# Kernel optimization log

Measured on AMD Instinct MI355X. Metric: run time of the kernel, lower is better.

## Reference

```python
import jax, jax.numpy as jnp
import numpy as np

B, S, D_IN, D_OUT, H = 2, 2048, 1024, 1024, 16
HD = D_OUT // H  # head dim = 64


def setup_inputs() -> dict:
    key = jax.random.key(0)
    ks = jax.random.split(key, 9)
    s_in = 1.0 / np.sqrt(D_IN)
    s_out = 1.0 / np.sqrt(D_OUT)
    return {
        "X": jax.random.normal(ks[0], (B, S, D_IN), dtype=jnp.float32),
        "Wq": jax.random.uniform(ks[1], (D_OUT, D_IN), jnp.float32, -s_in, s_in),
        "bq": jax.random.uniform(ks[2], (D_OUT,), jnp.float32, -s_in, s_in),
        "Wk": jax.random.uniform(ks[3], (D_OUT, D_IN), jnp.float32, -s_in, s_in),
        "bk": jax.random.uniform(ks[4], (D_OUT,), jnp.float32, -s_in, s_in),
        "Wv": jax.random.uniform(ks[5], (D_OUT, D_IN), jnp.float32, -s_in, s_in),
        "bv": jax.random.uniform(ks[6], (D_OUT,), jnp.float32, -s_in, s_in),
        "Wo": jax.random.uniform(ks[7], (D_OUT, D_OUT), jnp.float32, -s_out, s_out),
        "bo": jax.random.uniform(ks[8], (D_OUT,), jnp.float32, -s_out, s_out),
    }


def reference(X, Wq, bq, Wk, bk, Wv, bv, Wo, bo):
    scale = jnp.asarray(HD ** 0.5, X.dtype)  # self.dim = sqrt(head_dim)
    q = X @ Wq.T + bq  # [B,S,D_OUT]
    k = X @ Wk.T + bk
    v = X @ Wv.T + bv
    # split heads: b s (h d) -> b h s d
    q = q.reshape(B, S, H, HD).transpose(0, 2, 1, 3)
    k = k.reshape(B, S, H, HD).transpose(0, 2, 1, 3)
    v = v.reshape(B, S, H, HD).transpose(0, 2, 1, 3)
    scores = jnp.einsum('bhsd,bhtd->bhst', q, k) / scale  # [B,H,S,S]
    causal = jnp.triu(jnp.ones((S, S), dtype=bool), k=1)
    scores = jnp.where(causal, -jnp.inf, scores)
    weights = jax.nn.softmax(scores, axis=-1)
    out = jnp.einsum('bhst,bhtd->bhsd', weights, v)  # [B,H,S,HD]
    out = out.transpose(0, 2, 1, 3).reshape(B, S, D_OUT)  # b h s d -> b s (h d)
    return out @ Wo.T + bo
```

## Files before the change

kernel.cpp:

```cpp
#include <hip/hip_runtime.h>
#include <hip/hip_bf16.h>

typedef __bf16 bf16_t;
typedef __bf16 bf16x8 __attribute__((ext_vector_type(8)));
typedef float  f32x4  __attribute__((ext_vector_type(4)));
typedef unsigned short ushort_t;

#define MFMA16(a, b, c) __builtin_amdgcn_mfma_f32_16x16x32_bf16((a), (b), (c), 0, 0, 0)
#define GLDS16(g, l) __builtin_amdgcn_global_load_lds( \
    (const __attribute__((address_space(1))) unsigned int*)(g), \
    (__attribute__((address_space(3))) unsigned int*)(l), 16, 0, 0)

#define WAITCNT_VM(n)  (0x0F70 | (n))
#define WAITCNT_LGKM0  0xC07F

#define MEMFENCE asm volatile("" ::: "memory")

#define SWZ(r) ((((r) >> 1) ^ ((r) >> 3)) & 3)

#define QSCALE 0.18033688f

__global__ __launch_bounds__(256) void cvt_all(
    const void* __restrict__ X,  const void* __restrict__ W0, const void* __restrict__ W1,
    const void* __restrict__ W2, const void* __restrict__ W3,
    const void* __restrict__ c0, const void* __restrict__ c1,
    const void* __restrict__ c2, const void* __restrict__ c3,
    bf16_t* __restrict__ Xb, bf16_t* __restrict__ Wb, float* __restrict__ biasF,
    int* __restrict__ flag)
{
    const int tid  = threadIdx.x;
    const int lane = tid & 63;
    const ushort_t u = ((const ushort_t*)X)[2 * lane];
    const int e = (u >> 7) & 0xFF;
    const int f = (__ballot(e >= 0xA0) != 0ull) ? 1 : 0;

    const int bid = blockIdx.x;
    if (bid >= 4096) {
        if (bid == 4096 && tid == 0) *flag = f;
        const int idx = ((bid - 4096) * 256 + tid) * 8;
        const int w = idx >> 10, off = idx & 1023;
        const void* src = (w == 0) ? c0 : (w == 1) ? c1 : (w == 2) ? c2 : c3;
        #pragma unroll
        for (int r = 0; r < 8; ++r)
            biasF[idx + r] = f ? ((const float*)src)[off + r]
                               : (float)((const bf16_t*)src)[off + r];
        return;
    }

    const long long i = (long long)bid * 2048 + tid * 8;
    const void* src;
    bf16_t* dst;
    long long off;
    if (i < 4194304) { src = X; dst = Xb; off = i; }
    else {
        const int w = (int)((i - 4194304) >> 20);
        off = (i - 4194304) & 1048575;
        src = (w == 0) ? W0 : (w == 1) ? W1 : (w == 2) ? W2 : W3;
        dst = Wb + (size_t)w * 1048576;
    }
    if (f) {
        const float* s = (const float*)src + off;
        const float4 a = *(const float4*)(s);
        const float4 b = *(const float4*)(s + 4);
        bf16x8 o;
        o[0] = (bf16_t)a.x; o[1] = (bf16_t)a.y; o[2] = (bf16_t)a.z; o[3] = (bf16_t)a.w;
        o[4] = (bf16_t)b.x; o[5] = (bf16_t)b.y; o[6] = (bf16_t)b.z; o[7] = (bf16_t)b.w;
        *(bf16x8*)(dst + off) = o;
    } else {
        *(bf16x8*)(dst + off) = *(const bf16x8*)((const bf16_t*)src + off);
    }
}

__global__ __launch_bounds__(512, 2) void gemm_qkv(
    const bf16_t* __restrict__ A,
    const bf16_t* __restrict__ Wst,
    const float* __restrict__ biasAll,
    bf16_t* __restrict__ C, bf16_t* __restrict__ Vt)
{
    __shared__ bf16_t Ash[4][256 * 32];
    __shared__ bf16_t Bsh[4][192 * 32];

    const int tid  = threadIdx.x;
    const int wid  = tid >> 6;
    const int lane = tid & 63;
    const int g    = lane >> 4;
    const int c    = lane & 15;

    const int m0 = blockIdx.x * 256;
    const int n0 = blockIdx.y * 192;

    const int srow = lane >> 2;
    const int sblk = (lane & 3) ^ ((lane >> 3) & 3);
    const bf16_t* Ag  = A   + (size_t)(m0 + wid * 32 + srow) * 1024 + sblk * 8;
    const bf16_t* Wg0 = Wst + (size_t)(n0 + wid * 16 + srow) * 1024 + sblk * 8;
    const bf16_t* Wg1 = Wst + (size_t)(n0 + 128 + wid * 16 + srow) * 1024 + sblk * 8;

    const int waveM = (wid >> 2) * 128;
    const int waveN = (wid & 3) * 48;
    const int fblk  = (g ^ ((c >> 1) & 3)) * 8;

    f32x4 acc[8][3] = {};

    auto stage = [&](int H) {
        const int buf = H & 3;
        GLDS16(Ag + H * 32,                      &Ash[buf][(wid * 32) * 32]);
        GLDS16(Ag + (size_t)16 * 1024 + H * 32,  &Ash[buf][(wid * 32 + 16) * 32]);
        GLDS16(Wg0 + H * 32,                     &Bsh[buf][(wid * 16) * 32]);
        if (wid < 4)
            GLDS16(Wg1 + H * 32,                 &Bsh[buf][(128 + wid * 16) * 32]);
    };

    stage(0); stage(1); stage(2);
    if (wid < 4) __builtin_amdgcn_s_waitcnt(WAITCNT_VM(8));
    else         __builtin_amdgcn_s_waitcnt(WAITCNT_VM(6));
    __builtin_amdgcn_s_barrier();
    MEMFENCE;

    #pragma unroll 4
    for (int H = 0; H < 32; ++H) {
        const int buf = H & 3;
        const bf16_t* As = Ash[buf];
        const bf16_t* Bs = Bsh[buf];

        bf16x8 bfr[3], af[8];
        #pragma unroll
        for (int j = 0; j < 3; ++j)
            bfr[j] = *(const bf16x8*)(&Bs[(waveN + j * 16 + c) * 32 + fblk]);
        #pragma unroll
        for (int i = 0; i < 8; ++i)
            af[i] = *(const bf16x8*)(&As[(waveM + i * 16 + c) * 32 + fblk]);

        if (H < 29) stage(H + 3);

        __builtin_amdgcn_s_setprio(1);
        #pragma unroll
        for (int i = 0; i < 8; ++i)
            #pragma unroll
            for (int j = 0; j < 3; ++j)
                acc[i][j] = MFMA16(af[i], bfr[j], acc[i][j]);
        __builtin_amdgcn_s_setprio(0);

        MEMFENCE;
        __builtin_amdgcn_s_waitcnt(WAITCNT_LGKM0);
        if (H < 29) {
            if (wid < 4) __builtin_amdgcn_s_waitcnt(WAITCNT_VM(8));
            else         __builtin_amdgcn_s_waitcnt(WAITCNT_VM(6));
        } else if (H == 29) {
            if (wid < 4) __builtin_amdgcn_s_waitcnt(WAITCNT_VM(4));
            else         __builtin_amdgcn_s_waitcnt(WAITCNT_VM(3));
        } else if (H == 30) {
            __builtin_amdgcn_s_waitcnt(WAITCNT_VM(0));
        }
        __builtin_amdgcn_s_barrier();
        MEMFENCE;
    }

    #pragma unroll
    for (int j = 0; j < 3; ++j) {
        const int cg0 = n0 + waveN + j * 16;
        const int col = cg0 + c;
        const float bv = biasAll[col];
        if (cg0 >= 2048) {
            const int hcol = col - 2048;
            const int h = hcol >> 6, d = hcol & 63;
            #pragma unroll
            for (int i = 0; i < 8; ++i) {
                const int row = m0 + waveM + i * 16 + g * 4;
                const int bb = row >> 11, s = row & 2047;
                bf16_t pk[4];
                #pragma unroll
                for (int r = 0; r < 4; ++r) pk[r] = (bf16_t)(acc[i][j][r] + bv);
                *(uint2*)(&Vt[(((size_t)bb * 16 + h) * 64 + d) * 2048 + s]) = *(uint2*)pk;
            }
        } else {
            const float os = (cg0 < 1024) ? QSCALE : 1.0f;
            #pragma unroll
            for (int i = 0; i < 8; ++i) {
                const int row = m0 + waveM + i * 16 + g * 4;
                #pragma unroll
                for (int r = 0; r < 4; ++r)
                    C[(size_t)(row + r) * 3072 + col] = (bf16_t)((acc[i][j][r] + bv) * os);
            }
        }
    }
}

template<int TM>
__global__ __launch_bounds__(256, 3) void gemm_nt(
    const bf16_t* __restrict__ A,
    const bf16_t* __restrict__ W0,
    const float* __restrict__ b0,
    void* __restrict__ C, int ldc,
    const int* __restrict__ flag, int is_out)
{
    constexpr int MI = TM / 32;
    __shared__ bf16_t Ash[2][TM * 32];
    __shared__ bf16_t Bsh[2][128 * 32];

    const int f32out = is_out ? *flag : 0;

    const int tid  = threadIdx.x;
    const int wid  = tid >> 6;
    const int lane = tid & 63;
    const int g    = lane >> 4;
    const int c    = lane & 15;

    const int m0  = blockIdx.x * TM;
    const int n0  = blockIdx.y * 128;
    const bf16_t* W  = W0;
    const float*  bs = b0;
    const int nw = n0 & 1023;

    const int srow = lane >> 2;
    const int sblk = (lane & 3) ^ ((lane >> 3) & 3);
    const bf16_t* Ag = A + (size_t)(m0 + wid * (TM / 4) + srow) * 1024 + sblk * 8;
    const bf16_t* Wg = W + (size_t)(nw + wid * 32 + srow) * 1024 + sblk * 8;

    const int waveM = (wid >> 1) * (TM / 2);
    const int waveN = (wid & 1) * 64;

    f32x4 acc[MI][4] = {};
    const int fblk = (g ^ ((c >> 1) & 3)) * 8;

    auto stage = [&](int t) {
        const int k0 = t * 32;
        const int buf = t & 1;
        bf16_t* As = &Ash[buf][(wid * (TM / 4)) * 32];
        bf16_t* Bs = &Bsh[buf][(wid * 32) * 32];
        GLDS16(Ag + k0, As);
        if (TM == 128) GLDS16(Ag + (size_t)16 * 1024 + k0, As + 16 * 32);
        GLDS16(Wg + k0, Bs);
        GLDS16(Wg + (size_t)16 * 1024 + k0, Bs + 16 * 32);
    };

    stage(0);
    __builtin_amdgcn_s_waitcnt(WAITCNT_VM(0));
    __builtin_amdgcn_s_barrier();
    MEMFENCE;

    #pragma unroll 2
    for (int k = 0; k < 32; ++k) {
        const int cur = k & 1;
        bf16x8 af[MI], bfr[4];
        #pragma unroll
        for (int i = 0; i < MI; ++i)
            af[i] = *(const bf16x8*)(&Ash[cur][(waveM + i * 16 + c) * 32 + fblk]);
        #pragma unroll
        for (int j = 0; j < 4; ++j)
            bfr[j] = *(const bf16x8*)(&Bsh[cur][(waveN + j * 16 + c) * 32 + fblk]);

        if (k < 31) stage(k + 1);

        __builtin_amdgcn_s_setprio(1);
        #pragma unroll
        for (int i = 0; i < MI; ++i)
            #pragma unroll
            for (int j = 0; j < 4; ++j)
                acc[i][j] = MFMA16(af[i], bfr[j], acc[i][j]);
        __builtin_amdgcn_s_setprio(0);

        MEMFENCE;
        __builtin_amdgcn_s_waitcnt(WAITCNT_LGKM0);
        if (k < 31) __builtin_amdgcn_s_waitcnt(WAITCNT_VM(0));
        __builtin_amdgcn_s_barrier();
        MEMFENCE;
    }

    #pragma unroll
    for (int j = 0; j < 4; ++j) {
        const int col = n0 + waveN + j * 16 + c;
        const float bv = bs[col & 1023];
        #pragma unroll
        for (int i = 0; i < MI; ++i) {
            const int row = m0 + waveM + i * 16 + g * 4;
            #pragma unroll
            for (int r = 0; r < 4; ++r) {
                const float val = acc[i][j][r] + bv;
                const size_t idx = (size_t)(row + r) * ldc + col;
                if (f32out) ((float*)C)[idx] = val;
                else        ((bf16_t*)C)[idx] = (bf16_t)val;
            }
        }
    }
}

__global__ __launch_bounds__(256, 4) void attn_kernel(
    const bf16_t* __restrict__ QKV, const bf16_t* __restrict__ Vt,
    bf16_t* __restrict__ O)
{
    __shared__ bf16_t Ksh[2][64][32];
    __shared__ bf16_t Vsh[2][64][32];
    __shared__ bf16_t Psh[4][16][72];

    const int tid  = threadIdx.x;
    const int wid  = tid >> 6;
    const int lane = tid & 63;
    const int g    = lane >> 4;
    const int c    = lane & 15;

    const int bh = blockIdx.y;
    const int b  = bh >> 4, h = bh & 15;
    const int qt = (bh < 16) ? blockIdx.x : (31 - blockIdx.x);
    const int q0 = qt * 64;
    const int nt = qt + 1;

    bf16x8 aq[2];
    {
        const bf16_t* qp = QKV + (size_t)(b * 2048 + q0 + wid * 16 + c) * 3072 + h * 64;
        aq[0] = *(const bf16x8*)(qp + g * 8);
        aq[1] = *(const bf16x8*)(qp + 32 + g * 8);
    }

    float li = 0.0f;
    f32x4 o2[4] = {};

    const int sr = tid >> 2;
    const int j4 = tid & 3;
    const bf16_t* Kg = QKV + (size_t)(b * 2048 + sr) * 3072 + 1024 + h * 64 + j4 * 8;
    const bf16_t* Vg = Vt + ((size_t)bh * 64 + sr) * 2048 + j4 * 8;

    const int sp = (j4 ^ SWZ(sr)) * 8;
    bf16_t* kd0 = &Ksh[0][sr][sp];
    bf16_t* kd1 = &Ksh[1][sr][sp];
    bf16_t* vd0 = &Vsh[0][sr][sp];
    bf16_t* vd1 = &Vsh[1][sr][sp];

    uint4 kr0 = *(const uint4*)(Kg);
    uint4 kr1 = *(const uint4*)(Kg + 32);
    uint4 vr0 = *(const uint4*)(Vg);
    uint4 vr1 = *(const uint4*)(Vg + 32);

    const int qg = q0 + wid * 16 + c;

    for (int jt = 0; jt < nt; ++jt) {
        *(uint4*)kd0 = kr0;
        *(uint4*)kd1 = kr1;
        *(uint4*)vd0 = vr0;
        *(uint4*)vd1 = vr1;
        __syncthreads();

        if (jt + 1 < nt) {
            const size_t ko = (size_t)(jt + 1) * 64 * 3072;
            kr0 = *(const uint4*)(Kg + ko);
            kr1 = *(const uint4*)(Kg + ko + 32);
            vr0 = *(const uint4*)(Vg + (jt + 1) * 64);
            vr1 = *(const uint4*)(Vg + (jt + 1) * 64 + 32);
        }

        f32x4 s[4] = {};
        __builtin_amdgcn_s_setprio(1);
        #pragma unroll
        for (int n = 0; n < 4; ++n)
            #pragma unroll
            for (int kb = 0; kb < 2; ++kb) {
                const int row = n * 16 + c;
                const bf16x8 kf = *(const bf16x8*)(&Ksh[kb][row][(g ^ SWZ(row)) * 8]);
                s[n] = MFMA16(kf, aq[kb], s[n]);
            }
        __builtin_amdgcn_s_setprio(0);

        if (jt == nt - 1) {
            const int j0 = jt * 64;
            #pragma unroll
            for (int n = 0; n < 4; ++n)
                #pragma unroll
                for (int r = 0; r < 4; ++r)
                    if (j0 + n * 16 + g * 4 + r > qg) s[n][r] = -1e30f;
        }

        #pragma unroll
        for (int n = 0; n < 4; ++n) {
            const float p0 = __builtin_amdgcn_exp2f(s[n][0]);
            const float p1 = __builtin_amdgcn_exp2f(s[n][1]);
            const float p2 = __builtin_amdgcn_exp2f(s[n][2]);
            const float p3 = __builtin_amdgcn_exp2f(s[n][3]);
            li += (p0 + p1) + (p2 + p3);
            union { bf16_t h[4]; uint2 u; } pk;
            pk.h[0] = (bf16_t)p0; pk.h[1] = (bf16_t)p1;
            pk.h[2] = (bf16_t)p2; pk.h[3] = (bf16_t)p3;
            const int pw = ((n ^ (c >> 2)) << 2) + (g ^ (c & 3));
            *(uint2*)(&Psh[wid][c][pw * 4]) = pk.u;
        }
        __builtin_amdgcn_wave_barrier();

        bf16x8 pb[2];
        #pragma unroll
        for (int kb = 0; kb < 2; ++kb) {
            const int n0  = 2 * kb + (g >> 1);
            const int gs  = (g & 1) * 2;
            const int base = ((n0 ^ (c >> 2)) << 2);
            const uint2 w0 = *(const uint2*)(&Psh[wid][c][(base + (gs ^ (c & 3))) * 4]);
            const uint2 w1 = *(const uint2*)(&Psh[wid][c][(base + ((gs + 1) ^ (c & 3))) * 4]);
            union { uint4 u; bf16x8 v; } cvt;
            cvt.u.x = w0.x; cvt.u.y = w0.y; cvt.u.z = w1.x; cvt.u.w = w1.y;
            pb[kb] = cvt.v;
        }

        __builtin_amdgcn_s_setprio(1);
        #pragma unroll
        for (int kb = 0; kb < 2; ++kb)
            #pragma unroll
            for (int dt = 0; dt < 4; ++dt) {
                const int row = dt * 16 + c;
                const bf16x8 vf = *(const bf16x8*)(&Vsh[kb][row][(g ^ SWZ(row)) * 8]);
                o2[dt] = MFMA16(vf, pb[kb], o2[dt]);
            }
        __builtin_amdgcn_s_setprio(0);
        __syncthreads();
    }

    li += __shfl_xor(li, 16, 64);
    li += __shfl_xor(li, 32, 64);
    const float inv = 1.0f / li;

    const size_t orow = (size_t)(b * 2048 + q0 + wid * 16 + c);
    #pragma unroll
    for (int dt = 0; dt < 4; ++dt) {
        union { bf16_t h[4]; uint2 u; } pk;
        #pragma unroll
        for (int r = 0; r < 4; ++r) pk.h[r] = (bf16_t)(o2[dt][r] * inv);
        *(uint2*)(&O[orow * 1024 + h * 64 + dt * 16 + g * 4]) = pk.u;
    }
}

extern "C" void kernel_launch(void* const* d_in, const int* in_sizes, int n_in,
                              void* d_out, int out_size, void* d_ws, size_t ws_size,
                              hipStream_t stream)
{
    const void* X  = d_in[0];
    const void* Wq = d_in[1];  const void* bq = d_in[2];
    const void* Wk = d_in[3];  const void* bk = d_in[4];
    const void* Wv = d_in[5];  const void* bv = d_in[6];
    const void* Wo = d_in[7];  const void* bo = d_in[8];

    int*    flag  = (int*)d_ws;
    float*  biasF = (float*)((char*)d_ws + 16);
    bf16_t* Xb    = (bf16_t*)((char*)d_ws + 16 + 16384);
    bf16_t* Wb    = Xb  + (size_t)4096 * 1024;
    bf16_t* QKV   = Wb  + (size_t)4 * 1024 * 1024;
    bf16_t* Vt    = QKV + (size_t)4096 * 3072;
    bf16_t* Ao    = Vt  + (size_t)4096 * 1024;

    const size_t MW = (size_t)1024 * 1024;

    cvt_all<<<4098, 256, 0, stream>>>(X, Wq, Wk, Wv, Wo, bq, bk, bv, bo,
                                      Xb, Wb, biasF, flag);

    gemm_qkv<<<dim3(16, 16), 512, 0, stream>>>(Xb, Wb, biasF, QKV, Vt);
    attn_kernel<<<dim3(32, 32), 256, 0, stream>>>(QKV, Vt, Ao);
    gemm_nt<64><<<dim3(64, 8), 256, 0, stream>>>(
        Ao, Wb + 3 * MW, biasF + 3072, d_out, 1024, flag, 1);
}
```

Measured before the change: 194.8 us.

## Rewrite output projection GEMM with 128x128 tiles, 512 threads, triple-buffered K=64 stages

Replaces the templated 64x128-tile output GEMM with a dedicated kernel using 128x128 tiles and 8 waves. It loads K in 64-wide stages into a three-deep LDS ring, keeping two stages in flight. The goal is to raise data reuse per tile and hide global-load latency with fewer barriers. The cost is a grid of only 256 blocks, which may underfill the device's CUs, plus much larger LDS use per block.

```diff
diff --git a/kernel.cpp b/kernel.cpp
--- a/kernel.cpp
+++ b/kernel.cpp
@@ -185,19 +185,17 @@
     }
 }
 
-template<int TM>
-__global__ __launch_bounds__(256, 3) void gemm_nt(
+__global__ __launch_bounds__(512, 1) void gemm_op(
     const bf16_t* __restrict__ A,
-    const bf16_t* __restrict__ W0,
-    const float* __restrict__ b0,
-    void* __restrict__ C, int ldc,
-    const int* __restrict__ flag, int is_out)
+    const bf16_t* __restrict__ W,
+    const float* __restrict__ bs,
+    void* __restrict__ C,
+    const int* __restrict__ flag)
 {
-    constexpr int MI = TM / 32;
-    __shared__ bf16_t Ash[2][TM * 32];
-    __shared__ bf16_t Bsh[2][128 * 32];
-
-    const int f32out = is_out ? *flag : 0;
+    __shared__ bf16_t As[3][2][128 * 32];
+    __shared__ bf16_t Bs[3][2][128 * 32];
+
+    const int f32out = *flag;
 
     const int tid  = threadIdx.x;
     const int wid  = tid >> 6;
@@ -205,78 +203,77 @@
     const int g    = lane >> 4;
     const int c    = lane & 15;
 
-    const int m0  = blockIdx.x * TM;
-    const int n0  = blockIdx.y * 128;
-    const bf16_t* W  = W0;
-    const float*  bs = b0;
-    const int nw = n0 & 1023;
+    const int m0 = blockIdx.x * 128;
+    const int n0 = blockIdx.y * 128;
 
     const int srow = lane >> 2;
     const int sblk = (lane & 3) ^ ((lane >> 3) & 3);
-    const bf16_t* Ag = A + (size_t)(m0 + wid * (TM / 4) + srow) * 1024 + sblk * 8;
-    const bf16_t* Wg = W + (size_t)(nw + wid * 32 + srow) * 1024 + sblk * 8;
-
-    const int waveM = (wid >> 1) * (TM / 2);
-    const int waveN = (wid & 1) * 64;
-
-    f32x4 acc[MI][4] = {};
-    const int fblk = (g ^ ((c >> 1) & 3)) * 8;
+    const bf16_t* Ag = A + (size_t)(m0 + wid * 16 + srow) * 1024 + sblk * 8;
+    const bf16_t* Wg = W + (size_t)(n0 + wid * 16 + srow) * 1024 + sblk * 8;
+
+    const int waveM = (wid >> 2) * 64;
+    const int waveN = (wid & 3) * 32;
+    const int fblk  = (g ^ ((c >> 1) & 3)) * 8;
+
+    f32x4 acc[4][2] = {};
 
     auto stage = [&](int t) {
-        const int k0 = t * 32;
-        const int buf = t & 1;
-        bf16_t* As = &Ash[buf][(wid * (TM / 4)) * 32];
-        bf16_t* Bs = &Bsh[buf][(wid * 32) * 32];
-        GLDS16(Ag + k0, As);
-        if (TM == 128) GLDS16(Ag + (size_t)16 * 1024 + k0, As + 16 * 32);
-        GLDS16(Wg + k0, Bs);
-        GLDS16(Wg + (size_t)16 * 1024 + k0, Bs + 16 * 32);
+        const int buf = t % 3;
+        const size_t k0 = (size_t)t * 64;
+        GLDS16(Ag + k0,      &As[buf][0][(wid * 16) * 32]);
+        GLDS16(Ag + k0 + 32, &As[buf][1][(wid * 16) * 32]);
+        GLDS16(Wg + k0,      &Bs[buf][0][(wid * 16) * 32]);
+        GLDS16(Wg + k0 + 32, &Bs[buf][1][(wid * 16) * 32]);
     };
 
-    stage(0);
-    __builtin_amdgcn_s_waitcnt(WAITCNT_VM(0));
+    stage(0); stage(1);
+    __builtin_amdgcn_s_waitcnt(WAITCNT_VM(4));
     __builtin_amdgcn_s_barrier();
     MEMFENCE;
 
-    #pragma unroll 2
-    for (int k = 0; k < 32; ++k) {
-        const int cur = k & 1;
-        bf16x8 af[MI], bfr[4];
-        #pragma unroll
-        for (int i = 0; i < MI; ++i)
-            af[i] = *(const bf16x8*)(&Ash[cur][(waveM + i * 16 + c) * 32 + fblk]);
-        #pragma unroll
-        for (int j = 0; j < 4; ++j)
-            bfr[j] = *(const bf16x8*)(&Bsh[cur][(waveN + j * 16 + c) * 32 + fblk]);
-
-        if (k < 31) stage(k + 1);
+    #pragma unroll 3
+    for (int s = 0; s < 16; ++s) {
+        const int buf = s % 3;
+
+        if (s < 14) stage(s + 2);
 
         __builtin_amdgcn_s_setprio(1);
         #pragma unroll
-        for (int i = 0; i < MI; ++i)
-            #pragma unroll
-            for (int j = 0; j < 4; ++j)
-                acc[i][j] = MFMA16(af[i], bfr[j], acc[i][j]);
+        for (int kh = 0; kh < 2; ++kh) {
+            bf16x8 af[4], bfr[2];
+            #pragma unroll
+            for (int i = 0; i < 4; ++i)
+                af[i] = *(const bf16x8*)(&As[buf][kh][(waveM + i * 16 + c) * 32 + fblk]);
+            #pragma unroll
+            for (int j = 0; j < 2; ++j)
+                bfr[j] = *(const bf16x8*)(&Bs[buf][kh][(waveN + j * 16 + c) * 32 + fblk]);
+            #pragma unroll
+            for (int i = 0; i < 4; ++i)
+                #pragma unroll
+                for (int j = 0; j < 2; ++j)
+                    acc[i][j] = MFMA16(af[i], bfr[j], acc[i][j]);
+        }
         __builtin_amdgcn_s_setprio(0);
 
         MEMFENCE;
         __builtin_amdgcn_s_waitcnt(WAITCNT_LGKM0);
-        if (k < 31) __builtin_amdgcn_s_waitcnt(WAITCNT_VM(0));
+        if (s < 14)       __builtin_amdgcn_s_waitcnt(WAITCNT_VM(4));
+        else if (s == 14) __builtin_amdgcn_s_waitcnt(WAITCNT_VM(0));
         __builtin_amdgcn_s_barrier();
         MEMFENCE;
     }
 
     #pragma unroll
-    for (int j = 0; j < 4; ++j) {
+    for (int j = 0; j < 2; ++j) {
         const int col = n0 + waveN + j * 16 + c;
-        const float bv = bs[col & 1023];
-        #pragma unroll
-        for (int i = 0; i < MI; ++i) {
+        const float bv = bs[col];
+        #pragma unroll
+        for (int i = 0; i < 4; ++i) {
             const int row = m0 + waveM + i * 16 + g * 4;
             #pragma unroll
             for (int r = 0; r < 4; ++r) {
                 const float val = acc[i][j][r] + bv;
-                const size_t idx = (size_t)(row + r) * ldc + col;
+                const size_t idx = (size_t)(row + r) * 1024 + col;
                 if (f32out) ((float*)C)[idx] = val;
                 else        ((bf16_t*)C)[idx] = (bf16_t)val;
             }
@@ -448,6 +445,6 @@
 
     gemm_qkv<<<dim3(16, 16), 512, 0, stream>>>(Xb, Wb, biasF, QKV, Vt);
     attn_kernel<<<dim3(32, 32), 256, 0, stream>>>(QKV, Vt, Ao);
-    gemm_nt<64><<<dim3(64, 8), 256, 0, stream>>>(
-        Ao, Wb + 3 * MW, biasF + 3072, d_out, 1024, flag, 1);
+    gemm_op<<<dim3(32, 8), 512, 0, stream>>>(
+        Ao, Wb + 3 * MW, biasF + 3072, d_out, flag);
 }
```

New measurement: 186.7 us, median of 2. -4.1%, faster.
